# Performance work log

Measured on AMD Instinct MI355X. Metric: run time of the kernel, lower is better.

The kernel has to match this reference:

```python
import jax, jax.numpy as jnp
import numpy as np

NUM_NODES = 40000
NUM_EDGES = 400000
DIM = 128
NUM_REL = 502  # num_relation * 2
NUM_HEAD = 1


def setup_inputs() -> dict:
    key = jax.random.key(0)
    ks = jax.random.split(key, 16)
    d = DIM
    return {
        "curr_stat": jax.random.normal(ks[0], (NUM_NODES, d), jnp.float32),
        "last_stat": jax.random.normal(ks[1], (NUM_NODES, d), jnp.float32),
        "relemb_weight": jax.random.normal(ks[2], (NUM_REL, d), jnp.float32),
        "selfrel_weight": jax.random.normal(ks[3], (1, d), jnp.float32),
        "Wq": jax.random.normal(ks[4], (2 * d, d), jnp.float32) * (1.0 / np.sqrt(2 * d)),
        "bq": jax.random.normal(ks[5], (d,), jnp.float32) * 0.02,
        "Wk": jax.random.normal(ks[6], (2 * d, d), jnp.float32) * (1.0 / np.sqrt(2 * d)),
        "bk": jax.random.normal(ks[7], (d,), jnp.float32) * 0.02,
        "Wv": jax.random.normal(ks[8], (d, d), jnp.float32) * (1.0 / np.sqrt(d)),
        "bv": jax.random.normal(ks[9], (d,), jnp.float32) * 0.02,
        "dyn_weight": jax.random.normal(ks[10], (d, d), jnp.float32) * (1.0 / np.sqrt(d)),
        "edge_index": jax.random.randint(ks[11], (2, NUM_EDGES), 0, NUM_NODES, jnp.int32),
        "edge_type": jax.random.randint(ks[12], (NUM_EDGES,), 0, NUM_REL, jnp.int32),
    }


def _segment_softmax(scores, seg, num_segments):
    # scores: [E, H]; softmax over edges sharing the same destination segment
    m = jax.ops.segment_max(scores, seg, num_segments=num_segments)  # [N, H]
    e = jnp.exp(scores - m[seg])
    s = jax.ops.segment_sum(e, seg, num_segments=num_segments)  # [N, H]
    return e / s[seg]


def reference(curr_stat, last_stat, relemb_weight, selfrel_weight,
              Wq, bq, Wk, bk, Wv, bv, dyn_weight,
              edge_index, edge_type):
    N, D = curr_stat.shape
    H = NUM_HEAD
    HD = D // H

    # append self-loop edges for every node, with the dedicated self-relation
    loop = jnp.arange(N, dtype=edge_index.dtype)
    src = jnp.concatenate([edge_index[0], loop])  # [E_total]
    dst = jnp.concatenate([edge_index[1], loop])  # [E_total]
    type_emb = jnp.concatenate(
        [relemb_weight[edge_type], jnp.broadcast_to(selfrel_weight, (N, D))], axis=0)

    E = src.shape[0]
    # linear projections (x @ W + b); torch Linear stores W transposed, same math
    q = (jnp.concatenate([curr_stat[dst], type_emb], -1) @ Wq + bq).reshape(E, H, HD)
    k = (jnp.concatenate([last_stat[src], type_emb], -1) @ Wk + bk).reshape(E, H, HD)
    v = (last_stat[src] @ Wv + bv).reshape(E, H, HD)

    attn = jnp.sum(q * k, axis=-1) / np.sqrt(HD).astype(np.float32)  # [E, H]

    dyn_prob = _segment_softmax(attn, dst, N)   # [E, H]
    sta_prob = _segment_softmax(-attn, dst, N)  # [E, H]

    counts = jax.ops.segment_sum(jnp.ones((E,), jnp.float32), dst, num_segments=N)
    denom = jnp.maximum(counts, 1.0)[:, None]  # scatter-mean denominator

    feat_dyn = jax.ops.segment_sum((dyn_prob[..., None] * v).reshape(E, D), dst,
                                   num_segments=N) / denom
    feat_sta = jax.ops.segment_sum((sta_prob[..., None] * v).reshape(E, D), dst,
                                   num_segments=N) / denom

    # stack (feat_sta, feat_dyn @ dyn_weight) -> [2, N, D]
    return jnp.stack([feat_sta, feat_dyn @ dyn_weight])
```

## Files before the change

### kernel.cpp

```cpp
#include <hip/hip_runtime.h>
#include <hip/hip_bf16.h>
#include <math.h>

#define DIMC 128

typedef __attribute__((ext_vector_type(8))) short short8;
typedef __attribute__((ext_vector_type(4))) float floatx4;

static __device__ __forceinline__ unsigned pk2(float lo, float hi) {
    __hip_bfloat162 h = __float22bfloat162_rn(make_float2(lo, hi));
    return *(unsigned*)&h;
}
static __device__ __forceinline__ unsigned short f2bf(float x) {
    union { float f; unsigned int u; } v; v.f = x;
    unsigned int r = v.u + 0x7FFFu + ((v.u >> 16) & 1u);
    return (unsigned short)(r >> 16);
}
static __device__ __forceinline__ float2 bf2f2(unsigned int u) {
    union { unsigned int i; float f; } a, b;
    a.i = u << 16; b.i = u & 0xFFFF0000u;
    return make_float2(a.f, b.f);
}

struct PrepArgs { const float* W[4]; unsigned short* F[4]; };

__global__ __launch_bounds__(64) void prep_wfrag(PrepArgs a)
{
    int mat = blockIdx.y;
    int ts  = blockIdx.x;
    int s = ts & 3, t = ts >> 2;
    int lane = threadIdx.x;
    int q = lane >> 4, c = lane & 15;
    const float* W = a.W[mat];
    unsigned short o[8];
    #pragma unroll
    for (int j = 0; j < 8; ++j)
        o[j] = f2bf(W[(long)(s * 32 + q * 8 + j) * DIMC + t * 16 + c]);
    uint4 u;
    u.x = (unsigned)o[0] | ((unsigned)o[1] << 16);
    u.y = (unsigned)o[2] | ((unsigned)o[3] << 16);
    u.z = (unsigned)o[4] | ((unsigned)o[5] << 16);
    u.w = (unsigned)o[6] | ((unsigned)o[7] << 16);
    ((uint4*)a.F[mat])[ts * 64 + lane] = u;
}

struct GemmM3 {
    const float*          Af[3];
    const unsigned short* Ab[3];
    const unsigned short* F[3];
    const float*          bias[3];
    float*                outf[3];
    unsigned short*       outb[3];
    int                   ostride[3];
    int                   ooff[3];
};

__global__ __launch_bounds__(256) void gemm_mfma(GemmM3 g, int M)
{
    const int which = blockIdx.y;
    const float*          __restrict__ Af   = g.Af[which];
    const unsigned short* __restrict__ Ab   = g.Ab[which];
    const unsigned short* __restrict__ F    = g.F[which];
    const float*          __restrict__ bias = g.bias[which];
    float*          __restrict__ outf = g.outf[which];
    unsigned short* __restrict__ outb = g.outb[which];
    const int ostride = g.ostride[which];
    const int ooff    = g.ooff[which];

    const int wave = threadIdx.x >> 6;
    const int lane = threadIdx.x & 63;
    const int q = lane >> 4, c = lane & 15;
    const int rowbase = blockIdx.x * 64 + wave * 16;

    short8 wf[8][4];
    const uint4* Fp = (const uint4*)F;
    #pragma unroll
    for (int t = 0; t < 8; ++t)
        #pragma unroll
        for (int s = 0; s < 4; ++s) {
            uint4 u = Fp[(t * 4 + s) * 64 + lane];
            wf[t][s] = *(short8*)&u;
        }

    floatx4 acc[8];
    #pragma unroll
    for (int t = 0; t < 8; ++t) {
        float b = bias ? bias[t * 16 + c] : 0.0f;
        acc[t] = (floatx4){b, b, b, b};
    }

    short8 af[4];
    if (Af) {
        const float* Ar = Af + (long)(rowbase + c) * DIMC + q * 8;
        #pragma unroll
        for (int s = 0; s < 4; ++s) {
            float4 x0 = *(const float4*)(Ar + s * 32);
            float4 x1 = *(const float4*)(Ar + s * 32 + 4);
            uint4 u;
            u.x = pk2(x0.x, x0.y);
            u.y = pk2(x0.z, x0.w);
            u.z = pk2(x1.x, x1.y);
            u.w = pk2(x1.z, x1.w);
            af[s] = *(short8*)&u;
        }
    } else {
        const unsigned short* Ar = Ab + (long)(rowbase + c) * DIMC + q * 8;
        #pragma unroll
        for (int s = 0; s < 4; ++s) {
            uint4 u = *(const uint4*)(Ar + s * 32);
            af[s] = *(short8*)&u;
        }
    }

    #pragma unroll
    for (int t = 0; t < 8; ++t)
        #pragma unroll
        for (int s = 0; s < 4; ++s)
            acc[t] = __builtin_amdgcn_mfma_f32_16x16x32_bf16(af[s], wf[t][s], acc[t], 0, 0, 0);

    if (outf) {
        #pragma unroll
        for (int t = 0; t < 8; ++t)
            #pragma unroll
            for (int r = 0; r < 4; ++r)
                outf[(long)(rowbase + q * 4 + r) * DIMC + t * 16 + c] = acc[t][r];
    } else {
        #pragma unroll
        for (int t = 0; t < 8; ++t)
            #pragma unroll
            for (int r = 0; r < 4; ++r) {
                float other = __shfl_xor(acc[t][r], 1);
                if ((lane & 1) == 0) {
                    unsigned word = pk2(acc[t][r], other);
                    ((unsigned*)outb)[((long)(rowbase + q * 4 + r) * 64 + t * 8 + (c >> 1))
                                      * (long)ostride + ooff] = word;
                }
            }
    }
}

__global__ __launch_bounds__(128) void rel_proj(
    const float* __restrict__ relemb, const float* __restrict__ selfrel,
    const float* __restrict__ Wq, const float* __restrict__ bq,
    const float* __restrict__ Wk, const float* __restrict__ bk,
    uint2* __restrict__ QKre, int R)
{
    int t = blockIdx.x;
    int c = threadIdx.x;
    const float* row = (t < R) ? (relemb + (long)t * DIMC) : selfrel;
    float aq = bq[c], ak = bk[c];
    for (int k = 0; k < DIMC; ++k) {
        float a = row[k];
        aq = fmaf(a, Wq[(long)(DIMC + k) * DIMC + c], aq);
        ak = fmaf(a, Wk[(long)(DIMC + k) * DIMC + c], ak);
    }
    float aqo = __shfl_xor(aq, 1);
    float ako = __shfl_xor(ak, 1);
    if ((c & 1) == 0)
        QKre[(long)t * 64 + (c >> 1)] = make_uint2(pk2(aq, aqo), pk2(ak, ako));
}

__global__ void zero_int(int* __restrict__ p, int n) {
    int i = blockIdx.x * blockDim.x + threadIdx.x;
    if (i < n) p[i] = 0;
}

__global__ void hist_kernel(const int* __restrict__ dst, int* __restrict__ deg, int E) {
    int e = blockIdx.x * blockDim.x + threadIdx.x;
    if (e < E) atomicAdd(&deg[dst[e]], 1);
}

__global__ __launch_bounds__(256) void partial_sums(const int* __restrict__ deg,
                                                    int* __restrict__ partial, int N)
{
    __shared__ int sh[256];
    int t = threadIdx.x;
    int beg = blockIdx.x * 1024 + t * 4;
    int s = 0;
    if (beg + 3 < N) { int4 v = *(const int4*)(deg + beg); s = v.x + v.y + v.z + v.w; }
    else { for (int j = 0; j < 4; ++j) if (beg + j < N) s += deg[beg + j]; }
    sh[t] = s;
    __syncthreads();
    for (int d = 128; d >= 1; d >>= 1) {
        if (t < d) sh[t] += sh[t + d];
        __syncthreads();
    }
    if (t == 0) partial[blockIdx.x] = sh[0];
}

__global__ __launch_bounds__(256) void scan_partials(int* __restrict__ partial, int nb)
{
    __shared__ int sh[256];
    int t = threadIdx.x;
    sh[t] = (t < nb) ? partial[t] : 0;
    __syncthreads();
    for (int d = 1; d < 256; d <<= 1) {
        int v = (t >= d) ? sh[t - d] : 0;
        __syncthreads();
        sh[t] += v;
        __syncthreads();
    }
    if (t < nb) partial[t] = (t == 0) ? 0 : sh[t - 1];
}

__global__ __launch_bounds__(256) void write_offsets(const int* __restrict__ deg,
                                                     const int* __restrict__ partial,
                                                     int* __restrict__ offs,
                                                     int* __restrict__ cursor, int N)
{
    __shared__ int sh[256];
    int t = threadIdx.x;
    int beg = blockIdx.x * 1024 + t * 4;
    int d0 = 0, d1 = 0, d2 = 0, d3 = 0;
    if (beg + 3 < N) { int4 v = *(const int4*)(deg + beg); d0 = v.x; d1 = v.y; d2 = v.z; d3 = v.w; }
    else {
        if (beg < N)     d0 = deg[beg];
        if (beg + 1 < N) d1 = deg[beg + 1];
        if (beg + 2 < N) d2 = deg[beg + 2];
        if (beg + 3 < N) d3 = deg[beg + 3];
    }
    int s = d0 + d1 + d2 + d3;
    sh[t] = s;
    __syncthreads();
    for (int d = 1; d < 256; d <<= 1) {
        int v = (t >= d) ? sh[t - d] : 0;
        __syncthreads();
        sh[t] += v;
        __syncthreads();
    }
    int base = partial[blockIdx.x] + sh[t] - s;
    int o0 = base, o1 = o0 + d0, o2 = o1 + d1, o3 = o2 + d2;
    if (beg < N)     { offs[beg]     = o0; cursor[beg]     = o0; }
    if (beg + 1 < N) { offs[beg + 1] = o1; cursor[beg + 1] = o1; }
    if (beg + 2 < N) { offs[beg + 2] = o2; cursor[beg + 2] = o2; }
    if (beg + 3 < N) { offs[beg + 3] = o3; cursor[beg + 3] = o3; }
}

__global__ void scatter_kernel(const int* __restrict__ src, const int* __restrict__ dst,
                               const int* __restrict__ etype, int* __restrict__ cursor,
                               int2* __restrict__ sedge, int E)
{
    int e = blockIdx.x * blockDim.x + threadIdx.x;
    if (e < E) {
        int d = dst[e];
        int p = atomicAdd(&cursor[d], 1);
        sedge[p] = make_int2(src[e], etype[e]);
    }
}

__global__ __launch_bounds__(256) void node_kernel(
    const float* __restrict__ Qn,
    const uint2* __restrict__ KV,
    const uint2* __restrict__ QKre,
    const int* __restrict__ offs, const int* __restrict__ deg,
    const int2* __restrict__ sedge,
    float* __restrict__ out_sta, unsigned* __restrict__ feat_dyn,
    int N, int R)
{
    int n = (blockIdx.x * blockDim.x + threadIdx.x) >> 6;
    int lane = threadIdx.x & 63;
    if (n >= N) return;

    const float cs = 0.08838834764831845f * 1.4426950408889634f;
    int base = offs[n];
    int dcnt = deg[n];

    float2 qn = ((const float2*)(Qn + (long)n * DIMC))[lane];

    uint2 kvs = KV[(unsigned)n * 64u + lane];
    uint2 qks = QKre[(unsigned)R * 64u + lane];
    float2 ks = bf2f2(kvs.x), vs = bf2f2(kvs.y);
    float2 qr = bf2f2(qks.x), kr = bf2f2(qks.y);
    float p = (qn.x + qr.x) * (ks.x + kr.x) + (qn.y + qr.y) * (ks.y + kr.y);
    #pragma unroll
    for (int m = 32; m >= 1; m >>= 1) p += __shfl_xor(p, m);
    float a_self = p * cs;

    float m_dyn = a_self, s_dyn = 1.0f;
    float m_sta = -a_self, s_sta = 1.0f;
    float2 accd = vs;
    float2 accs = vs;

    int i = 0;
    for (; i + 4 <= dcnt; i += 4) {
        int2 e0 = sedge[base + i],     e1 = sedge[base + i + 1];
        int2 e2 = sedge[base + i + 2], e3 = sedge[base + i + 3];

        uint2 kv0 = KV[(unsigned)e0.x * 64u + lane];
        uint2 kv1 = KV[(unsigned)e1.x * 64u + lane];
        uint2 kv2 = KV[(unsigned)e2.x * 64u + lane];
        uint2 kv3 = KV[(unsigned)e3.x * 64u + lane];
        uint2 t0 = QKre[(unsigned)e0.y * 64u + lane];
        uint2 t1 = QKre[(unsigned)e1.y * 64u + lane];
        uint2 t2 = QKre[(unsigned)e2.y * 64u + lane];
        uint2 t3 = QKre[(unsigned)e3.y * 64u + lane];

        float2 kn0 = bf2f2(kv0.x), v0 = bf2f2(kv0.y);
        float2 kn1 = bf2f2(kv1.x), v1 = bf2f2(kv1.y);
        float2 kn2 = bf2f2(kv2.x), v2 = bf2f2(kv2.y);
        float2 kn3 = bf2f2(kv3.x), v3 = bf2f2(kv3.y);
        float2 q0 = bf2f2(t0.x), k0 = bf2f2(t0.y);
        float2 q1 = bf2f2(t1.x), k1 = bf2f2(t1.y);
        float2 q2 = bf2f2(t2.x), k2 = bf2f2(t2.y);
        float2 q3 = bf2f2(t3.x), k3 = bf2f2(t3.y);

        float p0 = (qn.x + q0.x) * (kn0.x + k0.x) + (qn.y + q0.y) * (kn0.y + k0.y);
        float p1 = (qn.x + q1.x) * (kn1.x + k1.x) + (qn.y + q1.y) * (kn1.y + k1.y);
        float p2 = (qn.x + q2.x) * (kn2.x + k2.x) + (qn.y + q2.y) * (kn2.y + k2.y);
        float p3 = (qn.x + q3.x) * (kn3.x + k3.x) + (qn.y + q3.y) * (kn3.y + k3.y);
        #pragma unroll
        for (int m = 32; m >= 1; m >>= 1) {
            p0 += __shfl_xor(p0, m);
            p1 += __shfl_xor(p1, m);
            p2 += __shfl_xor(p2, m);
            p3 += __shfl_xor(p3, m);
        }
        float a0 = p0 * cs, a1 = p1 * cs, a2 = p2 * cs, a3 = p3 * cs;

        float mx = fmaxf(fmaxf(a0, a1), fmaxf(a2, a3));
        float mn = fmaxf(m_dyn, mx);
        float f  = exp2f(m_dyn - mn);
        float w0 = exp2f(a0 - mn), w1 = exp2f(a1 - mn);
        float w2 = exp2f(a2 - mn), w3 = exp2f(a3 - mn);
        s_dyn = fmaf(s_dyn, f, (w0 + w1) + (w2 + w3));
        accd.x = fmaf(accd.x, f, fmaf(w0, v0.x, fmaf(w1, v1.x, fmaf(w2, v2.x, w3 * v3.x))));
        accd.y = fmaf(accd.y, f, fmaf(w0, v0.y, fmaf(w1, v1.y, fmaf(w2, v2.y, w3 * v3.y))));
        m_dyn = mn;

        float nmx = -fminf(fminf(a0, a1), fminf(a2, a3));
        float ms = fmaxf(m_sta, nmx);
        float fs = exp2f(m_sta - ms);
        float u0 = exp2f(-a0 - ms), u1 = exp2f(-a1 - ms);
        float u2 = exp2f(-a2 - ms), u3 = exp2f(-a3 - ms);
        s_sta = fmaf(s_sta, fs, (u0 + u1) + (u2 + u3));
        accs.x = fmaf(accs.x, fs, fmaf(u0, v0.x, fmaf(u1, v1.x, fmaf(u2, v2.x, u3 * v3.x))));
        accs.y = fmaf(accs.y, fs, fmaf(u0, v0.y, fmaf(u1, v1.y, fmaf(u2, v2.y, u3 * v3.y))));
        m_sta = ms;
    }

    for (; i < dcnt; ++i) {
        int2 e = sedge[base + i];
        uint2 kv = KV[(unsigned)e.x * 64u + lane];
        uint2 tt = QKre[(unsigned)e.y * 64u + lane];
        float2 kn = bf2f2(kv.x), v = bf2f2(kv.y);
        float2 q2 = bf2f2(tt.x), k2 = bf2f2(tt.y);
        float pp = (qn.x + q2.x) * (kn.x + k2.x) + (qn.y + q2.y) * (kn.y + k2.y);
        #pragma unroll
        for (int m = 32; m >= 1; m >>= 1) pp += __shfl_xor(pp, m);
        float a = pp * cs;

        float mn = fmaxf(m_dyn, a);
        float fd = exp2f(m_dyn - mn);
        float wd = exp2f(a - mn);
        s_dyn = fmaf(s_dyn, fd, wd);
        accd.x = fmaf(accd.x, fd, wd * v.x);
        accd.y = fmaf(accd.y, fd, wd * v.y);
        m_dyn = mn;

        float ms = fmaxf(m_sta, -a);
        float fs = exp2f(m_sta - ms);
        float ws_ = exp2f(-a - ms);
        s_sta = fmaf(s_sta, fs, ws_);
        accs.x = fmaf(accs.x, fs, ws_ * v.x);
        accs.y = fmaf(accs.y, fs, ws_ * v.y);
        m_sta = ms;
    }

    float denom = (float)(dcnt + 1);
    float id_ = 1.0f / (s_dyn * denom);
    float is_ = 1.0f / (s_sta * denom);
    ((float2*)(out_sta + (long)n * DIMC))[lane] = make_float2(accs.x * is_, accs.y * is_);
    feat_dyn[(unsigned)n * 64u + lane] = pk2(accd.x * id_, accd.y * id_);
}

extern "C" void kernel_launch(void* const* d_in, const int* in_sizes, int n_in,
                              void* d_out, int out_size, void* d_ws, size_t ws_size,
                              hipStream_t stream)
{
    const float* curr    = (const float*)d_in[0];
    const float* last    = (const float*)d_in[1];
    const float* relemb  = (const float*)d_in[2];
    const float* selfrel = (const float*)d_in[3];
    const float* Wq      = (const float*)d_in[4];
    const float* bq      = (const float*)d_in[5];
    const float* Wk      = (const float*)d_in[6];
    const float* bk      = (const float*)d_in[7];
    const float* Wv      = (const float*)d_in[8];
    const float* bv      = (const float*)d_in[9];
    const float* dynw    = (const float*)d_in[10];
    const int*   eidx    = (const int*)d_in[11];
    const int*   etype   = (const int*)d_in[12];
    float* out = (float*)d_out;

    const int N = in_sizes[0] / DIMC;
    const int E = in_sizes[12];
    const int R = in_sizes[2] / DIMC;
    const int* esrc = eidx;
    const int* edst = eidx + E;

    char* wp = (char*)d_ws;
    auto alloc = [&](size_t bytes) { char* r = wp; wp += (bytes + 15) & ~(size_t)15; return r; };
    size_t nd = (size_t)N * DIMC;
    float*          Qn    = (float*)alloc(nd * 4);
    uint2*          KV    = (uint2*)alloc((size_t)N * 64 * 8);
    unsigned short* Fdb   = (unsigned short*)alloc(nd * 2);
    uint2*          QKre  = (uint2*)alloc((size_t)(R + 1) * 64 * 8);
    unsigned short* FWq   = (unsigned short*)alloc(2048 * 8 * 2);
    unsigned short* FWk   = (unsigned short*)alloc(2048 * 8 * 2);
    unsigned short* FWv   = (unsigned short*)alloc(2048 * 8 * 2);
    unsigned short* FWd   = (unsigned short*)alloc(2048 * 8 * 2);
    int*            deg   = (int*)alloc((size_t)N * 4);
    int*            offs  = (int*)alloc((size_t)N * 4);
    int*            cursor= (int*)alloc((size_t)N * 4);
    int2*           sedge = (int2*)alloc((size_t)E * 8);
    int*            partial = (int*)alloc(256 * 4);

    const int gblk = N / 64;
    const int sblk = (N + 1023) / 1024;

    PrepArgs pa;
    pa.W[0] = Wq;   pa.F[0] = FWq;
    pa.W[1] = Wk;   pa.F[1] = FWk;
    pa.W[2] = Wv;   pa.F[2] = FWv;
    pa.W[3] = dynw; pa.F[3] = FWd;
    hipLaunchKernelGGL(prep_wfrag, dim3(32, 4), dim3(64), 0, stream, pa);

    GemmM3 qkv;
    qkv.Af[0] = curr; qkv.Ab[0] = nullptr; qkv.F[0] = FWq; qkv.bias[0] = nullptr;
    qkv.outf[0] = Qn; qkv.outb[0] = nullptr; qkv.ostride[0] = 1; qkv.ooff[0] = 0;
    qkv.Af[1] = last; qkv.Ab[1] = nullptr; qkv.F[1] = FWk; qkv.bias[1] = nullptr;
    qkv.outf[1] = nullptr; qkv.outb[1] = (unsigned short*)KV; qkv.ostride[1] = 2; qkv.ooff[1] = 0;
    qkv.Af[2] = last; qkv.Ab[2] = nullptr; qkv.F[2] = FWv; qkv.bias[2] = bv;
    qkv.outf[2] = nullptr; qkv.outb[2] = (unsigned short*)KV; qkv.ostride[2] = 2; qkv.ooff[2] = 1;
    hipLaunchKernelGGL(gemm_mfma, dim3(gblk, 3), dim3(256), 0, stream, qkv, N);

    hipLaunchKernelGGL(rel_proj, dim3(R + 1), dim3(128), 0, stream,
                       relemb, selfrel, Wq, bq, Wk, bk, QKre, R);
    hipLaunchKernelGGL(zero_int, dim3((N + 255) / 256), dim3(256), 0, stream, deg, N);
    hipLaunchKernelGGL(hist_kernel, dim3((E + 255) / 256), dim3(256), 0, stream, edst, deg, E);
    hipLaunchKernelGGL(partial_sums, dim3(sblk), dim3(256), 0, stream, deg, partial, N);
    hipLaunchKernelGGL(scan_partials, dim3(1), dim3(256), 0, stream, partial, sblk);
    hipLaunchKernelGGL(write_offsets, dim3(sblk), dim3(256), 0, stream,
                       deg, partial, offs, cursor, N);
    hipLaunchKernelGGL(scatter_kernel, dim3((E + 255) / 256), dim3(256), 0, stream,
                       esrc, edst, etype, cursor, sedge, E);
    hipLaunchKernelGGL(node_kernel, dim3((N + 3) / 4), dim3(256), 0, stream,
                       Qn, KV, QKre, offs, deg, sedge, out, (unsigned*)Fdb, N, R);

    GemmM3 fin;
    fin.Af[0] = nullptr; fin.Ab[0] = Fdb; fin.F[0] = FWd; fin.bias[0] = nullptr;
    fin.outf[0] = out + nd; fin.outb[0] = nullptr; fin.ostride[0] = 1; fin.ooff[0] = 0;
    fin.Af[1] = nullptr; fin.Ab[1] = Fdb; fin.F[1] = FWd; fin.bias[1] = nullptr;
    fin.outf[1] = out + nd; fin.outb[1] = nullptr; fin.ostride[1] = 1; fin.ooff[1] = 0;
    fin.Af[2] = nullptr; fin.Ab[2] = Fdb; fin.F[2] = FWd; fin.bias[2] = nullptr;
    fin.outf[2] = out + nd; fin.outb[2] = nullptr; fin.ostride[2] = 1; fin.ooff[2] = 0;
    hipLaunchKernelGGL(gemm_mfma, dim3(gblk, 1), dim3(256), 0, stream, fin, N);
}
```

Baseline: 243.0 us.

## Merge CSR build into cooperative kernel and fold relation projection into MFMA GEMM

Replaces the separate zero, histogram, partial-sum, scan, offset and scatter kernels with one cooperative kernel that uses grid-wide syncs, and folds the zeroing of degrees into a combined prep kernel. The relation-embedding Q/K projection moves from a scalar FMA kernel into the batched MFMA GEMM as two extra row-bounded slices. The aim is to cut kernel-launch count and the serial scalar rel_proj cost. In exchange it adds grid.sync barriers over 80 large blocks and bf16 rounding of the relation projections.

```diff
diff --git a/kernel.cpp b/kernel.cpp
--- a/kernel.cpp
+++ b/kernel.cpp
@@ -1,11 +1,14 @@
 #include <hip/hip_runtime.h>
 #include <hip/hip_bf16.h>
+#include <hip/hip_cooperative_groups.h>
 #include <math.h>
 
 #define DIMC 128
 
 typedef __attribute__((ext_vector_type(8))) short short8;
 typedef __attribute__((ext_vector_type(4))) float floatx4;
+
+namespace cg = cooperative_groups;
 
 static __device__ __forceinline__ unsigned pk2(float lo, float hi) {
     __hip_bfloat162 h = __float22bfloat162_rn(make_float2(lo, hi));
@@ -21,43 +24,67 @@
     a.i = u << 16; b.i = u & 0xFFFF0000u;
     return make_float2(a.f, b.f);
 }
-
-struct PrepArgs { const float* W[4]; unsigned short* F[4]; };
-
-__global__ __launch_bounds__(64) void prep_wfrag(PrepArgs a)
+static __device__ __forceinline__ int aload(const int* p) {
+    return __hip_atomic_load(p, __ATOMIC_RELAXED, __HIP_MEMORY_SCOPE_AGENT);
+}
+
+struct PrepArgs {
+    const float* W[6];
+    unsigned short* F[6];
+    const float* relemb; const float* selfrel;
+    float* TypeEmb;
+    int* deg;
+    int R; int N;
+};
+
+__global__ __launch_bounds__(64) void prep_all(PrepArgs a)
 {
-    int mat = blockIdx.y;
-    int ts  = blockIdx.x;
-    int s = ts & 3, t = ts >> 2;
+    int b = blockIdx.x;
     int lane = threadIdx.x;
-    int q = lane >> 4, c = lane & 15;
-    const float* W = a.W[mat];
-    unsigned short o[8];
-    #pragma unroll
-    for (int j = 0; j < 8; ++j)
-        o[j] = f2bf(W[(long)(s * 32 + q * 8 + j) * DIMC + t * 16 + c]);
-    uint4 u;
-    u.x = (unsigned)o[0] | ((unsigned)o[1] << 16);
-    u.y = (unsigned)o[2] | ((unsigned)o[3] << 16);
-    u.z = (unsigned)o[4] | ((unsigned)o[5] << 16);
-    u.w = (unsigned)o[6] | ((unsigned)o[7] << 16);
-    ((uint4*)a.F[mat])[ts * 64 + lane] = u;
-}
-
-struct GemmM3 {
-    const float*          Af[3];
-    const unsigned short* Ab[3];
-    const unsigned short* F[3];
-    const float*          bias[3];
-    float*                outf[3];
-    unsigned short*       outb[3];
-    int                   ostride[3];
-    int                   ooff[3];
+    if (b < 192) {
+        int mat = b >> 5, ts = b & 31;
+        int s = ts & 3, t = ts >> 2;
+        int q = lane >> 4, c = lane & 15;
+        const float* W = a.W[mat];
+        unsigned short o[8];
+        #pragma unroll
+        for (int j = 0; j < 8; ++j)
+            o[j] = f2bf(W[(long)(s * 32 + q * 8 + j) * DIMC + t * 16 + c]);
+        uint4 u;
+        u.x = (unsigned)o[0] | ((unsigned)o[1] << 16);
+        u.y = (unsigned)o[2] | ((unsigned)o[3] << 16);
+        u.z = (unsigned)o[4] | ((unsigned)o[5] << 16);
+        u.w = (unsigned)o[6] | ((unsigned)o[7] << 16);
+        ((uint4*)a.F[mat])[ts * 64 + lane] = u;
+    } else if (b < 192 + a.R + 1) {
+        int r = b - 192;
+        const float* src = (r < a.R) ? (a.relemb + (long)r * DIMC) : a.selfrel;
+        float2 v = ((const float2*)src)[lane];
+        ((float2*)(a.TypeEmb + (long)r * DIMC))[lane] = v;
+    } else {
+        int i = (b - (192 + a.R + 1)) * 64 + lane;
+        if (i < a.N) a.deg[i] = 0;
+    }
+}
+
+struct GemmM5 {
+    const float*          Af[5];
+    const unsigned short* Ab[5];
+    const unsigned short* F[5];
+    const float*          bias[5];
+    float*                outf[5];
+    unsigned short*       outb[5];
+    int                   ostride[5];
+    int                   ooff[5];
+    int                   M[5];
 };
 
-__global__ __launch_bounds__(256) void gemm_mfma(GemmM3 g, int M)
+__global__ __launch_bounds__(256) void gemm_mfma(GemmM5 g)
 {
     const int which = blockIdx.y;
+    const int M = g.M[which];
+    if (blockIdx.x * 64 >= M) return;
+
     const float*          __restrict__ Af   = g.Af[which];
     const unsigned short* __restrict__ Ab   = g.Ab[which];
     const unsigned short* __restrict__ F    = g.F[which];
@@ -89,9 +116,10 @@
         acc[t] = (floatx4){b, b, b, b};
     }
 
+    int rowA = rowbase + c; if (rowA > M - 1) rowA = M - 1;
     short8 af[4];
     if (Af) {
-        const float* Ar = Af + (long)(rowbase + c) * DIMC + q * 8;
+        const float* Ar = Af + (long)rowA * DIMC + q * 8;
         #pragma unroll
         for (int s = 0; s < 4; ++s) {
             float4 x0 = *(const float4*)(Ar + s * 32);
@@ -104,7 +132,7 @@
             af[s] = *(short8*)&u;
         }
     } else {
-        const unsigned short* Ar = Ab + (long)(rowbase + c) * DIMC + q * 8;
+        const unsigned short* Ar = Ab + (long)rowA * DIMC + q * 8;
         #pragma unroll
         for (int s = 0; s < 4; ++s) {
             uint4 u = *(const uint4*)(Ar + s * 32);
@@ -122,129 +150,102 @@
         #pragma unroll
         for (int t = 0; t < 8; ++t)
             #pragma unroll
-            for (int r = 0; r < 4; ++r)
-                outf[(long)(rowbase + q * 4 + r) * DIMC + t * 16 + c] = acc[t][r];
+            for (int r = 0; r < 4; ++r) {
+                int row = rowbase + q * 4 + r;
+                if (row < M)
+                    outf[(long)row * DIMC + t * 16 + c] = acc[t][r];
+            }
     } else {
         #pragma unroll
         for (int t = 0; t < 8; ++t)
             #pragma unroll
             for (int r = 0; r < 4; ++r) {
                 float other = __shfl_xor(acc[t][r], 1);
-                if ((lane & 1) == 0) {
+                int row = rowbase + q * 4 + r;
+                if ((lane & 1) == 0 && row < M) {
                     unsigned word = pk2(acc[t][r], other);
-                    ((unsigned*)outb)[((long)(rowbase + q * 4 + r) * 64 + t * 8 + (c >> 1))
+                    ((unsigned*)outb)[((long)row * 64 + t * 8 + (c >> 1))
                                       * (long)ostride + ooff] = word;
                 }
             }
     }
 }
 
-__global__ __launch_bounds__(128) void rel_proj(
-    const float* __restrict__ relemb, const float* __restrict__ selfrel,
-    const float* __restrict__ Wq, const float* __restrict__ bq,
-    const float* __restrict__ Wk, const float* __restrict__ bk,
-    uint2* __restrict__ QKre, int R)
+struct CsrArgs {
+    const int* esrc; const int* edst; const int* etype;
+    int* deg; int* offs; int* cursor;
+    int* partial; int* baseArr;
+    int2* sedge;
+    int N; int E; int nblk;
+};
+
+__global__ __launch_bounds__(1024) void csr_coop(CsrArgs a)
 {
-    int t = blockIdx.x;
-    int c = threadIdx.x;
-    const float* row = (t < R) ? (relemb + (long)t * DIMC) : selfrel;
-    float aq = bq[c], ak = bk[c];
-    for (int k = 0; k < DIMC; ++k) {
-        float a = row[k];
-        aq = fmaf(a, Wq[(long)(DIMC + k) * DIMC + c], aq);
-        ak = fmaf(a, Wk[(long)(DIMC + k) * DIMC + c], ak);
-    }
-    float aqo = __shfl_xor(aq, 1);
-    float ako = __shfl_xor(ak, 1);
-    if ((c & 1) == 0)
-        QKre[(long)t * 64 + (c >> 1)] = make_uint2(pk2(aq, aqo), pk2(ak, ako));
-}
-
-__global__ void zero_int(int* __restrict__ p, int n) {
-    int i = blockIdx.x * blockDim.x + threadIdx.x;
-    if (i < n) p[i] = 0;
-}
-
-__global__ void hist_kernel(const int* __restrict__ dst, int* __restrict__ deg, int E) {
-    int e = blockIdx.x * blockDim.x + threadIdx.x;
-    if (e < E) atomicAdd(&deg[dst[e]], 1);
-}
-
-__global__ __launch_bounds__(256) void partial_sums(const int* __restrict__ deg,
-                                                    int* __restrict__ partial, int N)
-{
-    __shared__ int sh[256];
-    int t = threadIdx.x;
-    int beg = blockIdx.x * 1024 + t * 4;
-    int s = 0;
-    if (beg + 3 < N) { int4 v = *(const int4*)(deg + beg); s = v.x + v.y + v.z + v.w; }
-    else { for (int j = 0; j < 4; ++j) if (beg + j < N) s += deg[beg + j]; }
-    sh[t] = s;
+    cg::grid_group grid = cg::this_grid();
+    const int b = blockIdx.x, t = threadIdx.x;
+    const int lane = t & 63, wid = t >> 6;
+    const int gsz = gridDim.x * 1024;
+
+    for (int e = b * 1024 + t; e < a.E; e += gsz)
+        atomicAdd(&a.deg[a.edst[e]], 1);
+    __threadfence();
+    grid.sync();
+
+    __shared__ int wsum[16], wbase[16];
+    int i = b * 1024 + t;
+    int d_i = (i < a.N) ? aload(&a.deg[i]) : 0;
+    int v = d_i;
+    #pragma unroll
+    for (int d = 1; d < 64; d <<= 1) {
+        int u = __shfl_up(v, d);
+        if (lane >= d) v += u;
+    }
+    if (lane == 63) wsum[wid] = v;
     __syncthreads();
-    for (int d = 128; d >= 1; d >>= 1) {
-        if (t < d) sh[t] += sh[t + d];
+    if (wid == 0 && lane < 16) {
+        int s = wsum[lane];
+        #pragma unroll
+        for (int d = 1; d < 16; d <<= 1) {
+            int u = __shfl_up(s, d);
+            if (lane >= d) s += u;
+        }
+        wbase[lane] = s - wsum[lane];
+        if (lane == 15) a.partial[b] = s;
+    }
+    __syncthreads();
+    int incl = v + wbase[wid];
+    int excl = incl - d_i;
+    __threadfence();
+    grid.sync();
+
+    if (b == 0) {
+        __shared__ int sb[128];
+        int val = (t < a.nblk) ? aload(&a.partial[t]) : 0;
+        if (t < 128) sb[t] = val;
         __syncthreads();
-    }
-    if (t == 0) partial[blockIdx.x] = sh[0];
-}
-
-__global__ __launch_bounds__(256) void scan_partials(int* __restrict__ partial, int nb)
-{
-    __shared__ int sh[256];
-    int t = threadIdx.x;
-    sh[t] = (t < nb) ? partial[t] : 0;
-    __syncthreads();
-    for (int d = 1; d < 256; d <<= 1) {
-        int v = (t >= d) ? sh[t - d] : 0;
-        __syncthreads();
-        sh[t] += v;
-        __syncthreads();
-    }
-    if (t < nb) partial[t] = (t == 0) ? 0 : sh[t - 1];
-}
-
-__global__ __launch_bounds__(256) void write_offsets(const int* __restrict__ deg,
-                                                     const int* __restrict__ partial,
-                                                     int* __restrict__ offs,
-                                                     int* __restrict__ cursor, int N)
-{
-    __shared__ int sh[256];
-    int t = threadIdx.x;
-    int beg = blockIdx.x * 1024 + t * 4;
-    int d0 = 0, d1 = 0, d2 = 0, d3 = 0;
-    if (beg + 3 < N) { int4 v = *(const int4*)(deg + beg); d0 = v.x; d1 = v.y; d2 = v.z; d3 = v.w; }
-    else {
-        if (beg < N)     d0 = deg[beg];
-        if (beg + 1 < N) d1 = deg[beg + 1];
-        if (beg + 2 < N) d2 = deg[beg + 2];
-        if (beg + 3 < N) d3 = deg[beg + 3];
-    }
-    int s = d0 + d1 + d2 + d3;
-    sh[t] = s;
-    __syncthreads();
-    for (int d = 1; d < 256; d <<= 1) {
-        int v = (t >= d) ? sh[t - d] : 0;
-        __syncthreads();
-        sh[t] += v;
-        __syncthreads();
-    }
-    int base = partial[blockIdx.x] + sh[t] - s;
-    int o0 = base, o1 = o0 + d0, o2 = o1 + d1, o3 = o2 + d2;
-    if (beg < N)     { offs[beg]     = o0; cursor[beg]     = o0; }
-    if (beg + 1 < N) { offs[beg + 1] = o1; cursor[beg + 1] = o1; }
-    if (beg + 2 < N) { offs[beg + 2] = o2; cursor[beg + 2] = o2; }
-    if (beg + 3 < N) { offs[beg + 3] = o3; cursor[beg + 3] = o3; }
-}
-
-__global__ void scatter_kernel(const int* __restrict__ src, const int* __restrict__ dst,
-                               const int* __restrict__ etype, int* __restrict__ cursor,
-                               int2* __restrict__ sedge, int E)
-{
-    int e = blockIdx.x * blockDim.x + threadIdx.x;
-    if (e < E) {
-        int d = dst[e];
-        int p = atomicAdd(&cursor[d], 1);
-        sedge[p] = make_int2(src[e], etype[e]);
+        for (int d = 1; d < 128; d <<= 1) {
+            int u = (t >= d && t < 128) ? sb[t - d] : 0;
+            __syncthreads();
+            if (t < 128) sb[t] += u;
+            __syncthreads();
+        }
+        if (t < a.nblk) a.baseArr[t] = sb[t] - val;
+    }
+    __threadfence();
+    grid.sync();
+
+    int bb = aload(&a.baseArr[b]);
+    if (i < a.N) {
+        a.offs[i]   = bb + excl;
+        a.cursor[i] = bb + excl;
+    }
+    __threadfence();
+    grid.sync();
+
+    for (int e = b * 1024 + t; e < a.E; e += gsz) {
+        int d = a.edst[e];
+        int p = atomicAdd(&a.cursor[d], 1);
+        a.sedge[p] = make_int2(a.esrc[e], a.etype[e]);
     }
 }
 
@@ -405,54 +406,55 @@
     uint2*          KV    = (uint2*)alloc((size_t)N * 64 * 8);
     unsigned short* Fdb   = (unsigned short*)alloc(nd * 2);
     uint2*          QKre  = (uint2*)alloc((size_t)(R + 1) * 64 * 8);
-    unsigned short* FWq   = (unsigned short*)alloc(2048 * 8 * 2);
-    unsigned short* FWk   = (unsigned short*)alloc(2048 * 8 * 2);
-    unsigned short* FWv   = (unsigned short*)alloc(2048 * 8 * 2);
-    unsigned short* FWd   = (unsigned short*)alloc(2048 * 8 * 2);
+    float*          TypeEmb = (float*)alloc((size_t)(R + 2) * DIMC * 4);
+    unsigned short* FW[6];
+    for (int m = 0; m < 6; ++m) FW[m] = (unsigned short*)alloc(2048 * 8 * 2);
     int*            deg   = (int*)alloc((size_t)N * 4);
     int*            offs  = (int*)alloc((size_t)N * 4);
     int*            cursor= (int*)alloc((size_t)N * 4);
     int2*           sedge = (int2*)alloc((size_t)E * 8);
-    int*            partial = (int*)alloc(256 * 4);
+    int*            partial = (int*)alloc(128 * 4);
+    int*            baseArr = (int*)alloc(128 * 4);
 
     const int gblk = N / 64;
-    const int sblk = (N + 1023) / 1024;
 
     PrepArgs pa;
-    pa.W[0] = Wq;   pa.F[0] = FWq;
-    pa.W[1] = Wk;   pa.F[1] = FWk;
-    pa.W[2] = Wv;   pa.F[2] = FWv;
-    pa.W[3] = dynw; pa.F[3] = FWd;
-    hipLaunchKernelGGL(prep_wfrag, dim3(32, 4), dim3(64), 0, stream, pa);
-
-    GemmM3 qkv;
-    qkv.Af[0] = curr; qkv.Ab[0] = nullptr; qkv.F[0] = FWq; qkv.bias[0] = nullptr;
-    qkv.outf[0] = Qn; qkv.outb[0] = nullptr; qkv.ostride[0] = 1; qkv.ooff[0] = 0;
-    qkv.Af[1] = last; qkv.Ab[1] = nullptr; qkv.F[1] = FWk; qkv.bias[1] = nullptr;
-    qkv.outf[1] = nullptr; qkv.outb[1] = (unsigned short*)KV; qkv.ostride[1] = 2; qkv.ooff[1] = 0;
-    qkv.Af[2] = last; qkv.Ab[2] = nullptr; qkv.F[2] = FWv; qkv.bias[2] = bv;
-    qkv.outf[2] = nullptr; qkv.outb[2] = (unsigned short*)KV; qkv.ostride[2] = 2; qkv.ooff[2] = 1;
-    hipLaunchKernelGGL(gemm_mfma, dim3(gblk, 3), dim3(256), 0, stream, qkv, N);
-
-    hipLaunchKernelGGL(rel_proj, dim3(R + 1), dim3(128), 0, stream,
-                       relemb, selfrel, Wq, bq, Wk, bk, QKre, R);
-    hipLaunchKernelGGL(zero_int, dim3((N + 255) / 256), dim3(256), 0, stream, deg, N);
-    hipLaunchKernelGGL(hist_kernel, dim3((E + 255) / 256), dim3(256), 0, stream, edst, deg, E);
-    hipLaunchKernelGGL(partial_sums, dim3(sblk), dim3(256), 0, stream, deg, partial, N);
-    hipLaunchKernelGGL(scan_partials, dim3(1), dim3(256), 0, stream, partial, sblk);
-    hipLaunchKernelGGL(write_offsets, dim3(sblk), dim3(256), 0, stream,
-                       deg, partial, offs, cursor, N);
-    hipLaunchKernelGGL(scatter_kernel, dim3((E + 255) / 256), dim3(256), 0, stream,
-                       esrc, edst, etype, cursor, sedge, E);
+    pa.W[0] = Wq;   pa.W[1] = Wk;   pa.W[2] = Wv;
+    pa.W[3] = dynw; pa.W[4] = Wq + (size_t)DIMC * DIMC; pa.W[5] = Wk + (size_t)DIMC * DIMC;
+    for (int m = 0; m < 6; ++m) pa.F[m] = FW[m];
+    pa.relemb = relemb; pa.selfrel = selfrel; pa.TypeEmb = TypeEmb;
+    pa.deg = deg; pa.R = R; pa.N = N;
+    int pgrid = 192 + (R + 1) + (N + 63) / 64;
+    hipLaunchKernelGGL(prep_all, dim3(pgrid), dim3(64), 0, stream, pa);
+
+    CsrArgs ca;
+    ca.esrc = esrc; ca.edst = edst; ca.etype = etype;
+    ca.deg = deg; ca.offs = offs; ca.cursor = cursor;
+    ca.partial = partial; ca.baseArr = baseArr; ca.sedge = sedge;
+    ca.N = N; ca.E = E; ca.nblk = 80;
+    void* cargs[] = { &ca };
+    hipLaunchCooperativeKernel((const void*)csr_coop, dim3(80), dim3(1024), cargs, 0, stream);
+
+    GemmM5 g5;
+    for (int s = 0; s < 5; ++s) { g5.Ab[s] = nullptr; g5.outf[s] = nullptr; g5.outb[s] = nullptr; }
+    g5.Af[0] = curr;    g5.F[0] = FW[0]; g5.bias[0] = nullptr; g5.outf[0] = Qn;
+    g5.ostride[0] = 1;  g5.ooff[0] = 0;  g5.M[0] = N;
+    g5.Af[1] = last;    g5.F[1] = FW[1]; g5.bias[1] = nullptr; g5.outb[1] = (unsigned short*)KV;
+    g5.ostride[1] = 2;  g5.ooff[1] = 0;  g5.M[1] = N;
+    g5.Af[2] = last;    g5.F[2] = FW[2]; g5.bias[2] = bv;      g5.outb[2] = (unsigned short*)KV;
+    g5.ostride[2] = 2;  g5.ooff[2] = 1;  g5.M[2] = N;
+    g5.Af[3] = TypeEmb; g5.F[3] = FW[4]; g5.bias[3] = bq;      g5.outb[3] = (unsigned short*)QKre;
+    g5.ostride[3] = 2;  g5.ooff[3] = 0;  g5.M[3] = R + 1;
+    g5.Af[4] = TypeEmb; g5.F[4] = FW[5]; g5.bias[4] = bk;      g5.outb[4] = (unsigned short*)QKre;
+    g5.ostride[4] = 2;  g5.ooff[4] = 1;  g5.M[4] = R + 1;
+    hipLaunchKernelGGL(gemm_mfma, dim3(gblk, 5), dim3(256), 0, stream, g5);
+
     hipLaunchKernelGGL(node_kernel, dim3((N + 3) / 4), dim3(256), 0, stream,
                        Qn, KV, QKre, offs, deg, sedge, out, (unsigned*)Fdb, N, R);
 
-    GemmM3 fin;
-    fin.Af[0] = nullptr; fin.Ab[0] = Fdb; fin.F[0] = FWd; fin.bias[0] = nullptr;
-    fin.outf[0] = out + nd; fin.outb[0] = nullptr; fin.ostride[0] = 1; fin.ooff[0] = 0;
-    fin.Af[1] = nullptr; fin.Ab[1] = Fdb; fin.F[1] = FWd; fin.bias[1] = nullptr;
-    fin.outf[1] = out + nd; fin.outb[1] = nullptr; fin.ostride[1] = 1; fin.ooff[1] = 0;
-    fin.Af[2] = nullptr; fin.Ab[2] = Fdb; fin.F[2] = FWd; fin.bias[2] = nullptr;
-    fin.outf[2] = out + nd; fin.outb[2] = nullptr; fin.ostride[2] = 1; fin.ooff[2] = 0;
-    hipLaunchKernelGGL(gemm_mfma, dim3(gblk, 1), dim3(256), 0, stream, fin, N);
-}
+    GemmM5 gf;
+    for (int s = 0; s < 5; ++s) { gf.Af[s] = nullptr; gf.Ab[s] = nullptr; gf.outf[s] = nullptr; gf.outb[s] = nullptr; gf.M[s] = 0; }
+    gf.Ab[0] = Fdb; gf.F[0] = FW[3]; gf.bias[0] = nullptr; gf.outf[0] = out + nd;
+    gf.ostride[0] = 1; gf.ooff[0] = 0; gf.M[0] = N;
+    hipLaunchKernelGGL(gemm_mfma, dim3(gblk, 1), dim3(256), 0, stream, gf);
+}
```

After: 386.8 us. 59.2% more time.
